# Kernel optimization log

Hardware: AMD Instinct MI355X
Metric: run time of the kernel (lower is better)

## Reference

```python
import jax, jax.numpy as jnp
import numpy as np

N = 262144   # collocation points
Q = 100      # IRK stages
H = 50       # hidden width (hardcoded in DNN)


def setup_inputs() -> dict:
    key = jax.random.key(0)
    ks = jax.random.split(key, 16)
    dims = [(1, H), (H, H), (H, H), (H, H), (H, H), (H, Q)]
    inp = {}
    for j, (i, o) in enumerate(dims):
        k1, k2 = jax.random.split(ks[j])
        s = 1.0 / np.sqrt(i)  # torch nn.Linear default init range
        inp[f"W{j}"] = jax.random.uniform(k1, (i, o), jnp.float32, -s, s)
        inp[f"b{j}"] = jax.random.uniform(k2, (o,), jnp.float32, -s, s)
    inp["x"] = jax.random.uniform(ks[10], (N, 1), jnp.float32, -1.0, 1.0)
    inp["lambda_1"] = jnp.array([0.0], jnp.float32)
    inp["lambda_2"] = jnp.array([-6.0], jnp.float32)
    inp["IRK_alpha"] = jax.random.uniform(ks[11], (Q, Q), jnp.float32) * 0.01
    inp["dt"] = jnp.float32(0.01)
    return inp


def reference(W0, b0, W1, b1, W2, b2, W3, b3, W4, b4, W5, b5,
              x, lambda_1, lambda_2, IRK_alpha, dt):
    def u_fn(xx):  # [N,1] -> [N,Q]
        h = xx
        for W, b in ((W0, b0), (W1, b1), (W2, b2), (W3, b3), (W4, b4)):
            h = jnp.tanh(h @ W + b)
        return h @ W5 + b5

    ones = jnp.ones_like(x)
    # u_x, u_xx via nested forward-mode (x is scalar per sample, so jvp with
    # tangent 1 gives the exact per-column derivative, same as the torch
    # double-autograd dummy trick).
    def u_and_ux(xx):
        return jax.jvp(u_fn, (xx,), (ones,))  # (u, u_x)

    (u, u_x), (_, u_xx) = jax.jvp(u_and_ux, (x,), (ones,))

    f = -lambda_1 * u * u_x + jnp.exp(lambda_2) * u_xx  # [N,Q]
    return u - dt * (f @ IRK_alpha.T)
```

## Files before the change

### kernel.cpp

```cpp
#include <hip/hip_runtime.h>
#include <hip/hip_bf16.h>


#define NPTS 262144
#define HW   50
#define Q    100
#define BLK  64
#define SPW  32
#define SPB  32
#define NBLK (NPTS / SPB)

#define WS_W5    65536
#define WS_W5AF  94208
#define WS_ALPHA 108544
#define WS_DENSE 137216

typedef float f32x4 __attribute__((ext_vector_type(4)));
typedef short bf16x8 __attribute__((ext_vector_type(8)));
typedef unsigned int u32x4 __attribute__((ext_vector_type(4)));

#define MFMA __builtin_amdgcn_mfma_f32_16x16x32_bf16

__device__ __forceinline__ unsigned int pack_bf2(float a, float b) {
    __hip_bfloat162 h = __float22bfloat162_rn(make_float2(a, b));
    unsigned int u;
    __builtin_memcpy(&u, &h, 4);
    return u;
}
__device__ __forceinline__ float lo_f(unsigned int p) {
    return __builtin_bit_cast(float, p << 16);
}
__device__ __forceinline__ float hi_f(unsigned int p) {
    return __builtin_bit_cast(float, p & 0xffff0000u);
}
__device__ __forceinline__ float fast_tanh(float z) {
    float e = __expf(2.0f * z);
    return 1.0f - __fdividef(2.0f, e + 1.0f);
}

__global__ void __launch_bounds__(256, 1)
compute_w5a(const float* __restrict__ W5, const float* __restrict__ alpha,
            float* __restrict__ w5a)
{
    int idx = blockIdx.x * 256 + threadIdx.x;
    if (idx >= HW * Q) return;
    int i = idx / Q, q = idx - i * Q;
    float acc = 0.0f;
    for (int j = 0; j < Q; ++j)
        acc = fmaf(W5[i * Q + j], alpha[q * Q + j], acc);
    w5a[idx] = acc;
}

__global__ void __launch_bounds__(64, 1)
build_frags(const float* __restrict__ W1, const float* __restrict__ W2,
            const float* __restrict__ W3, const float* __restrict__ W4,
            const float* __restrict__ W5, const float* __restrict__ alpha,
            unsigned char* __restrict__ ws)
{
    const int ln  = threadIdx.x;
    const int fid = blockIdx.x;

    const float* src;
    int ld, kmax, mmax, kt, mt;
    bool trans, isLo;
    size_t dst;

    if (fid < 64) {
        int L = fid >> 4, f = fid & 15;
        src = (L == 0) ? W1 : (L == 1) ? W2 : (L == 2) ? W3 : W4;
        ld = HW; kmax = HW; mmax = HW; trans = true;
        isLo = f >= 8;
        int ff = f & 7;
        kt = ff >> 2; mt = ff & 3;
        dst = (size_t)(L * 16384 + f * 1024);
    } else if (fid < 92) {
        int f = fid - 64;
        src = W5; ld = Q; kmax = HW; mmax = Q; trans = true;
        isLo = f >= 14;
        int ff = isLo ? f - 14 : f;
        kt = ff / 7; mt = ff % 7;
        dst = (size_t)(WS_W5 + f * 1024);
    } else if (fid < 106) {
        int f = fid - 92;
        src = (const float*)(ws + WS_DENSE);
        ld = Q; kmax = HW; mmax = Q; trans = true;
        isLo = false;
        kt = f / 7; mt = f % 7;
        dst = (size_t)(WS_W5AF + f * 1024);
    } else {
        int f = fid - 106;
        src = alpha; ld = Q; kmax = Q; mmax = Q; trans = false;
        isLo = false;
        kt = f / 7; mt = f % 7;
        dst = (size_t)(WS_ALPHA + f * 1024);
    }

    int m  = mt * 16 + (ln & 15);
    int kb = kt * 32 + (ln >> 4) * 8;
    bool mv = (m < mmax);
    unsigned int wout[4];
#pragma unroll
    for (int jj = 0; jj < 4; ++jj) {
        int k0 = kb + 2 * jj, k1 = k0 + 1;
        float v0 = (mv && k0 < kmax) ? (trans ? src[k0 * ld + m] : src[m * ld + k0]) : 0.0f;
        float v1 = (mv && k1 < kmax) ? (trans ? src[k1 * ld + m] : src[m * ld + k1]) : 0.0f;
        unsigned int h = pack_bf2(v0, v1);
        if (isLo)
            wout[jj] = pack_bf2(v0 - lo_f(h), v1 - hi_f(h));
        else
            wout[jj] = h;
    }
    *(uint4*)(ws + dst + ln * 16) = make_uint4(wout[0], wout[1], wout[2], wout[3]);
}

__global__ void __launch_bounds__(BLK, 2)
pinn_mfma(const float* __restrict__ b0v, const float* __restrict__ W0,
          const float* __restrict__ b1, const float* __restrict__ b2,
          const float* __restrict__ b3, const float* __restrict__ b4,
          const float* __restrict__ b5,
          const float* __restrict__ x, const float* __restrict__ lam1p,
          const float* __restrict__ lam2p, const float* __restrict__ dtp,
          const unsigned char* __restrict__ ws, float* __restrict__ out)
{
    __shared__ __align__(16) unsigned char statebuf[8192];

    const int lane = threadIdx.x & 63;
    const int l15  = lane & 15;
    const int g    = lane >> 4;
    const int sbase = blockIdx.x * SPB;

    unsigned char* st0 = &statebuf[0];
    unsigned char* st1 = &statebuf[4096];
    const unsigned char* wgl = ws + lane * 16;
    const int swz = (l15 & 7) << 4;

    const f32x4 Z4 = {0.0f, 0.0f, 0.0f, 0.0f};

    bf16x8 Bh_hi[2][2], Bh_lo[2][2], Bx[2][2], Bxx[2][2];

    {
        float xv[2];
        xv[0] = x[sbase + l15];
        xv[1] = x[sbase + 16 + l15];
#pragma unroll
        for (int kt = 0; kt < 2; ++kt) {
            float wv[8], bv[8];
#pragma unroll
            for (int j = 0; j < 8; ++j) {
                int ch = kt * 32 + g * 8 + j;
                wv[j] = (ch < HW) ? W0[ch] : 0.0f;
                bv[j] = (ch < HW) ? b0v[ch] : 0.0f;
            }
#pragma unroll
            for (int nt = 0; nt < 2; ++nt) {
                u32x4 uh, ul, ux, uxx;
#pragma unroll
                for (int jp = 0; jp < 4; ++jp) {
                    float t0 = fast_tanh(fmaf(xv[nt], wv[2*jp],   bv[2*jp]));
                    float t1 = fast_tanh(fmaf(xv[nt], wv[2*jp+1], bv[2*jp+1]));
                    float s0 = 1.0f - t0 * t0, s1 = 1.0f - t1 * t1;
                    float hx0 = s0 * wv[2*jp],   hx1 = s1 * wv[2*jp+1];
                    float hxx0 = -2.0f * t0 * hx0 * wv[2*jp];
                    float hxx1 = -2.0f * t1 * hx1 * wv[2*jp+1];
                    unsigned int h = pack_bf2(t0, t1);
                    uh[jp]  = h;
                    ul[jp]  = pack_bf2(t0 - lo_f(h), t1 - hi_f(h));
                    ux[jp]  = pack_bf2(hx0, hx1);
                    uxx[jp] = pack_bf2(hxx0, hxx1);
                }
                Bh_hi[kt][nt] = __builtin_bit_cast(bf16x8, uh);
                Bh_lo[kt][nt] = __builtin_bit_cast(bf16x8, ul);
                Bx[kt][nt]    = __builtin_bit_cast(bf16x8, ux);
                Bxx[kt][nt]   = __builtin_bit_cast(bf16x8, uxx);
            }
        }
    }

    for (int L = 0; L < 4; ++L) {
        const float* bl = (L == 0) ? b1 : (L == 1) ? b2 : (L == 2) ? b3 : b4;
        const unsigned char* wfl = wgl + L * 16384;

        float bb[4][4];
#pragma unroll
        for (int mt = 0; mt < 4; ++mt)
#pragma unroll
            for (int r = 0; r < 4; ++r) {
                int ch = mt * 16 + g * 4 + r;
                bb[mt][r] = (ch < HW) ? bl[ch] : 0.0f;
            }

        f32x4 at[4][2], ax[4][2], axx[4][2];
#pragma unroll
        for (int mt = 0; mt < 4; ++mt)
#pragma unroll
            for (int nt = 0; nt < 2; ++nt) {
#pragma unroll
                for (int r = 0; r < 4; ++r) at[mt][nt][r] = bb[mt][r];
                ax[mt][nt] = Z4; axx[mt][nt] = Z4;
            }

#pragma unroll
        for (int kt = 0; kt < 2; ++kt) {
#pragma unroll
            for (int mt = 0; mt < 4; ++mt) {
                bf16x8 Ahi = *(const bf16x8*)(wfl + (kt * 4 + mt) * 1024);
                bf16x8 Alo = *(const bf16x8*)(wfl + (8 + kt * 4 + mt) * 1024);
#pragma unroll
                for (int nt = 0; nt < 2; ++nt) {
                    at[mt][nt]  = MFMA(Ahi, Bh_hi[kt][nt], at[mt][nt], 0, 0, 0);
                    at[mt][nt]  = MFMA(Ahi, Bh_lo[kt][nt], at[mt][nt], 0, 0, 0);
                    at[mt][nt]  = MFMA(Alo, Bh_hi[kt][nt], at[mt][nt], 0, 0, 0);
                    ax[mt][nt]  = MFMA(Ahi, Bx[kt][nt],  ax[mt][nt],  0, 0, 0);
                    axx[mt][nt] = MFMA(Ahi, Bxx[kt][nt], axx[mt][nt], 0, 0, 0);
                }
            }
        }

#pragma unroll
        for (int mt = 0; mt < 4; ++mt)
#pragma unroll
            for (int nt = 0; nt < 2; ++nt) {
                float t0 = fast_tanh(at[mt][nt][0]);
                float t1 = fast_tanh(at[mt][nt][1]);
                float t2 = fast_tanh(at[mt][nt][2]);
                float t3 = fast_tanh(at[mt][nt][3]);
                at[mt][nt][0] = t0; at[mt][nt][1] = t1;
                at[mt][nt][2] = t2; at[mt][nt][3] = t3;
                unsigned int h0 = pack_bf2(t0, t1);
                unsigned int h1 = pack_bf2(t2, t3);
                unsigned int l0 = pack_bf2(t0 - lo_f(h0), t1 - hi_f(h0));
                unsigned int l1 = pack_bf2(t2 - lo_f(h1), t3 - hi_f(h1));
                int off = ((nt * 16 + l15) * 128 + (mt * 16 + g * 4) * 2) ^ swz;
                *(uint2*)(st0 + off) = make_uint2(h0, h1);
                *(uint2*)(st1 + off) = make_uint2(l0, l1);
            }
#pragma unroll
        for (int kt = 0; kt < 2; ++kt)
#pragma unroll
            for (int nt = 0; nt < 2; ++nt) {
                int off = ((nt * 16 + l15) * 128 + (kt * 32 + g * 8) * 2) ^ swz;
                Bh_hi[kt][nt] = *(const bf16x8*)(st0 + off);
                Bh_lo[kt][nt] = *(const bf16x8*)(st1 + off);
            }
        asm volatile("s_waitcnt lgkmcnt(0)" ::: "memory");

#pragma unroll
        for (int mt = 0; mt < 4; ++mt)
#pragma unroll
            for (int nt = 0; nt < 2; ++nt) {
                float hx[4], hxx[4];
#pragma unroll
                for (int r = 0; r < 4; ++r) {
                    float t   = at[mt][nt][r];
                    float s   = fmaf(-t, t, 1.0f);
                    float zx  = ax[mt][nt][r];
                    float zxx = axx[mt][nt][r];
                    hx[r]  = s * zx;
                    hxx[r] = fmaf(s, zxx, -2.0f * t * zx * hx[r]);
                }
                unsigned int a0 = pack_bf2(hx[0], hx[1]);
                unsigned int a1 = pack_bf2(hx[2], hx[3]);
                unsigned int c0 = pack_bf2(hxx[0], hxx[1]);
                unsigned int c1 = pack_bf2(hxx[2], hxx[3]);
                int off = ((nt * 16 + l15) * 128 + (mt * 16 + g * 4) * 2) ^ swz;
                *(uint2*)(st0 + off) = make_uint2(a0, a1);
                *(uint2*)(st1 + off) = make_uint2(c0, c1);
            }
#pragma unroll
        for (int kt = 0; kt < 2; ++kt)
#pragma unroll
            for (int nt = 0; nt < 2; ++nt) {
                int off = ((nt * 16 + l15) * 128 + (kt * 32 + g * 8) * 2) ^ swz;
                Bx[kt][nt]  = *(const bf16x8*)(st0 + off);
                Bxx[kt][nt] = *(const bf16x8*)(st1 + off);
            }
        asm volatile("s_waitcnt lgkmcnt(0)" ::: "memory");
    }

    const float lam1 = lam1p[0];
    const float el2  = __expf(lam2p[0]);
    const float dtv  = dtp[0];

    const unsigned char* w5f = wgl + WS_W5;

    if (lam1 == 0.0f) {
        const unsigned char* waf = wgl + WS_W5AF;
        const float c = dtv * el2;
#pragma unroll
        for (int mt = 0; mt < 7; ++mt) {
            f32x4 au[2], acr[2];
#pragma unroll
            for (int nt = 0; nt < 2; ++nt) {
#pragma unroll
                for (int r = 0; r < 4; ++r) {
                    int q = mt * 16 + g * 4 + r;
                    au[nt][r] = (q < Q) ? b5[q] : 0.0f;
                }
                acr[nt] = Z4;
            }
#pragma unroll
            for (int kt = 0; kt < 2; ++kt) {
                bf16x8 Ahi = *(const bf16x8*)(w5f + (kt * 7 + mt) * 1024);
                bf16x8 Alo = *(const bf16x8*)(w5f + (14 + kt * 7 + mt) * 1024);
                bf16x8 Aa  = *(const bf16x8*)(waf + (kt * 7 + mt) * 1024);
#pragma unroll
                for (int nt = 0; nt < 2; ++nt) {
                    au[nt]  = MFMA(Ahi, Bh_hi[kt][nt], au[nt],  0, 0, 0);
                    au[nt]  = MFMA(Ahi, Bh_lo[kt][nt], au[nt],  0, 0, 0);
                    au[nt]  = MFMA(Alo, Bh_hi[kt][nt], au[nt],  0, 0, 0);
                    acr[nt] = MFMA(Aa,  Bxx[kt][nt],   acr[nt], 0, 0, 0);
                }
            }
#pragma unroll
            for (int nt = 0; nt < 2; ++nt) {
                int s = nt * 16 + l15;
                f32x4 ov;
#pragma unroll
                for (int r = 0; r < 4; ++r)
                    ov[r] = fmaf(-c, acr[nt][r], au[nt][r]);
                *(f32x4*)(st0 + s * 64 + g * 16) = ov;
            }
            asm volatile("s_waitcnt lgkmcnt(0)" ::: "memory");
#pragma unroll
            for (int p = 0; p < 2; ++p) {
                int s  = p * 16 + (lane >> 2);
                int qi = (lane & 3) * 4;
                f32x4 v = *(const f32x4*)(st0 + s * 64 + qi * 4);
                int qb = mt * 16 + qi;
                if (qb < Q)
                    *(f32x4*)(&out[(size_t)(sbase + s) * Q + qb]) = v;
            }
            asm volatile("s_waitcnt lgkmcnt(0)" ::: "memory");
        }
    } else {
        f32x4 u_all[7][2];
#pragma unroll
        for (int mt = 0; mt < 7; ++mt) {
            f32x4 au[2], aux_[2], auxx[2];
#pragma unroll
            for (int nt = 0; nt < 2; ++nt) {
#pragma unroll
                for (int r = 0; r < 4; ++r) {
                    int q = mt * 16 + g * 4 + r;
                    au[nt][r] = (q < Q) ? b5[q] : 0.0f;
                }
                aux_[nt] = Z4; auxx[nt] = Z4;
            }
#pragma unroll
            for (int kt = 0; kt < 2; ++kt) {
                bf16x8 Ahi = *(const bf16x8*)(w5f + (kt * 7 + mt) * 1024);
                bf16x8 Alo = *(const bf16x8*)(w5f + (14 + kt * 7 + mt) * 1024);
#pragma unroll
                for (int nt = 0; nt < 2; ++nt) {
                    au[nt]   = MFMA(Ahi, Bh_hi[kt][nt], au[nt],   0, 0, 0);
                    au[nt]   = MFMA(Ahi, Bh_lo[kt][nt], au[nt],   0, 0, 0);
                    au[nt]   = MFMA(Alo, Bh_hi[kt][nt], au[nt],   0, 0, 0);
                    aux_[nt] = MFMA(Ahi, Bx[kt][nt],  aux_[nt], 0, 0, 0);
                    auxx[nt] = MFMA(Ahi, Bxx[kt][nt], auxx[nt], 0, 0, 0);
                }
            }
#pragma unroll
            for (int nt = 0; nt < 2; ++nt) {
                float fv[4];
#pragma unroll
                for (int r = 0; r < 4; ++r) {
                    int q = mt * 16 + g * 4 + r;
                    float u = au[nt][r];
                    u_all[mt][nt][r] = u;
                    float f = fmaf(-lam1 * u, aux_[nt][r], el2 * auxx[nt][r]);
                    fv[r] = (q < Q) ? f : 0.0f;
                }
                unsigned int f0 = pack_bf2(fv[0], fv[1]);
                unsigned int f1 = pack_bf2(fv[2], fv[3]);
                int s = nt * 16 + l15;
                int off = (s * 256 + (mt * 16 + g * 4) * 2) ^ swz;
                *(uint2*)(st0 + off) = make_uint2(f0, f1);
            }
        }

        bf16x8 Ff[4][2];
#pragma unroll
        for (int kt = 0; kt < 4; ++kt)
#pragma unroll
            for (int nt = 0; nt < 2; ++nt) {
                int s = nt * 16 + l15;
                int off = (s * 256 + (kt * 32 + g * 8) * 2) ^ swz;
                Ff[kt][nt] = *(const bf16x8*)(st0 + off);
            }
        asm volatile("s_waitcnt lgkmcnt(0)" ::: "memory");
        {
            const bf16x8 z8 = {0, 0, 0, 0, 0, 0, 0, 0};
            if (g >= 2) { Ff[3][0] = z8; Ff[3][1] = z8; }
        }

        const unsigned char* alf = wgl + WS_ALPHA;
#pragma unroll
        for (int mt = 0; mt < 7; ++mt) {
            f32x4 ac[2]; ac[0] = Z4; ac[1] = Z4;
#pragma unroll
            for (int kt = 0; kt < 4; ++kt) {
                bf16x8 Aa = *(const bf16x8*)(alf + (kt * 7 + mt) * 1024);
#pragma unroll
                for (int nt = 0; nt < 2; ++nt)
                    ac[nt] = MFMA(Aa, Ff[kt][nt], ac[nt], 0, 0, 0);
            }
#pragma unroll
            for (int nt = 0; nt < 2; ++nt) {
                int s = nt * 16 + l15;
                f32x4 ov;
#pragma unroll
                for (int r = 0; r < 4; ++r)
                    ov[r] = fmaf(-dtv, ac[nt][r], u_all[mt][nt][r]);
                *(f32x4*)(st0 + s * 64 + g * 16) = ov;
            }
            asm volatile("s_waitcnt lgkmcnt(0)" ::: "memory");
#pragma unroll
            for (int p = 0; p < 2; ++p) {
                int s  = p * 16 + (lane >> 2);
                int qi = (lane & 3) * 4;
                f32x4 v = *(const f32x4*)(st0 + s * 64 + qi * 4);
                int qb = mt * 16 + qi;
                if (qb < Q)
                    *(f32x4*)(&out[(size_t)(sbase + s) * Q + qb]) = v;
            }
            asm volatile("s_waitcnt lgkmcnt(0)" ::: "memory");
        }
    }
}

extern "C" void kernel_launch(void* const* d_in, const int* in_sizes, int n_in,
                              void* d_out, int out_size, void* d_ws, size_t ws_size,
                              hipStream_t stream) {
    const float* W0 = (const float*)d_in[0];
    const float* b0 = (const float*)d_in[1];
    const float* W1 = (const float*)d_in[2];
    const float* b1 = (const float*)d_in[3];
    const float* W2 = (const float*)d_in[4];
    const float* b2 = (const float*)d_in[5];
    const float* W3 = (const float*)d_in[6];
    const float* b3 = (const float*)d_in[7];
    const float* W4 = (const float*)d_in[8];
    const float* b4 = (const float*)d_in[9];
    const float* W5 = (const float*)d_in[10];
    const float* b5 = (const float*)d_in[11];
    const float* x     = (const float*)d_in[12];
    const float* lam1  = (const float*)d_in[13];
    const float* lam2  = (const float*)d_in[14];
    const float* alpha = (const float*)d_in[15];
    const float* dt    = (const float*)d_in[16];

    unsigned char* ws = (unsigned char*)d_ws;

    compute_w5a<<<20, 256, 0, stream>>>(W5, alpha, (float*)(ws + WS_DENSE));
    build_frags<<<134, 64, 0, stream>>>(W1, W2, W3, W4, W5, alpha, ws);
    pinn_mfma<<<NBLK, BLK, 0, stream>>>(b0, W0, b1, b2, b3, b4, b5,
                                        x, lam1, lam2, dt,
                                        (const unsigned char*)ws, (float*)d_out);
}
```

Measured before the change: 124.7 us.

## Restructure hidden layers per M-tile with four LDS staging buffers

Reorders each hidden layer so every 16-channel M-tile does its MFMAs, tanh and derivative epilogue before the next tile starts. This cuts live accumulators from 24 f32x4 to 6 and lowers register pressure. The h, h_lo, h_x and h_xx tiles now go to four separate LDS buffers, doubling shared memory to 16KB, and are reloaded with a single wait instead of two. The extra LDS per block could limit occupancy, and the per-tile MFMA chains are shorter with less independent work to interleave.

```diff
diff --git a/kernel.cpp b/kernel.cpp
--- a/kernel.cpp
+++ b/kernel.cpp
@@ -122,15 +122,17 @@
           const float* __restrict__ lam2p, const float* __restrict__ dtp,
           const unsigned char* __restrict__ ws, float* __restrict__ out)
 {
-    __shared__ __align__(16) unsigned char statebuf[8192];
+    __shared__ __align__(16) unsigned char statebuf[16384];
 
     const int lane = threadIdx.x & 63;
     const int l15  = lane & 15;
     const int g    = lane >> 4;
     const int sbase = blockIdx.x * SPB;
 
-    unsigned char* st0 = &statebuf[0];
-    unsigned char* st1 = &statebuf[4096];
+    unsigned char* stHh  = &statebuf[0];
+    unsigned char* stHl  = &statebuf[4096];
+    unsigned char* stHx  = &statebuf[8192];
+    unsigned char* stHxx = &statebuf[12288];
     const unsigned char* wgl = ws + lane * 16;
     const int swz = (l15 & 7) << 4;
 
@@ -180,99 +182,68 @@
         const float* bl = (L == 0) ? b1 : (L == 1) ? b2 : (L == 2) ? b3 : b4;
         const unsigned char* wfl = wgl + L * 16384;
 
-        float bb[4][4];
-#pragma unroll
-        for (int mt = 0; mt < 4; ++mt)
-#pragma unroll
-            for (int r = 0; r < 4; ++r) {
-                int ch = mt * 16 + g * 4 + r;
-                bb[mt][r] = (ch < HW) ? bl[ch] : 0.0f;
-            }
-
-        f32x4 at[4][2], ax[4][2], axx[4][2];
-#pragma unroll
-        for (int mt = 0; mt < 4; ++mt)
-#pragma unroll
-            for (int nt = 0; nt < 2; ++nt) {
-#pragma unroll
-                for (int r = 0; r < 4; ++r) at[mt][nt][r] = bb[mt][r];
-                ax[mt][nt] = Z4; axx[mt][nt] = Z4;
-            }
-
-#pragma unroll
-        for (int kt = 0; kt < 2; ++kt) {
-#pragma unroll
-            for (int mt = 0; mt < 4; ++mt) {
+#pragma unroll
+        for (int mt = 0; mt < 4; ++mt) {
+            f32x4 at[2], ax[2], axx[2];
+#pragma unroll
+            for (int nt = 0; nt < 2; ++nt) {
+#pragma unroll
+                for (int r = 0; r < 4; ++r) {
+                    int ch = mt * 16 + g * 4 + r;
+                    at[nt][r] = (ch < HW) ? bl[ch] : 0.0f;
+                }
+                ax[nt] = Z4; axx[nt] = Z4;
+            }
+#pragma unroll
+            for (int kt = 0; kt < 2; ++kt) {
                 bf16x8 Ahi = *(const bf16x8*)(wfl + (kt * 4 + mt) * 1024);
                 bf16x8 Alo = *(const bf16x8*)(wfl + (8 + kt * 4 + mt) * 1024);
 #pragma unroll
                 for (int nt = 0; nt < 2; ++nt) {
-                    at[mt][nt]  = MFMA(Ahi, Bh_hi[kt][nt], at[mt][nt], 0, 0, 0);
-                    at[mt][nt]  = MFMA(Ahi, Bh_lo[kt][nt], at[mt][nt], 0, 0, 0);
-                    at[mt][nt]  = MFMA(Alo, Bh_hi[kt][nt], at[mt][nt], 0, 0, 0);
-                    ax[mt][nt]  = MFMA(Ahi, Bx[kt][nt],  ax[mt][nt],  0, 0, 0);
-                    axx[mt][nt] = MFMA(Ahi, Bxx[kt][nt], axx[mt][nt], 0, 0, 0);
-                }
-            }
-        }
-
-#pragma unroll
-        for (int mt = 0; mt < 4; ++mt)
-#pragma unroll
-            for (int nt = 0; nt < 2; ++nt) {
-                float t0 = fast_tanh(at[mt][nt][0]);
-                float t1 = fast_tanh(at[mt][nt][1]);
-                float t2 = fast_tanh(at[mt][nt][2]);
-                float t3 = fast_tanh(at[mt][nt][3]);
-                at[mt][nt][0] = t0; at[mt][nt][1] = t1;
-                at[mt][nt][2] = t2; at[mt][nt][3] = t3;
-                unsigned int h0 = pack_bf2(t0, t1);
-                unsigned int h1 = pack_bf2(t2, t3);
-                unsigned int l0 = pack_bf2(t0 - lo_f(h0), t1 - hi_f(h0));
-                unsigned int l1 = pack_bf2(t2 - lo_f(h1), t3 - hi_f(h1));
-                int off = ((nt * 16 + l15) * 128 + (mt * 16 + g * 4) * 2) ^ swz;
-                *(uint2*)(st0 + off) = make_uint2(h0, h1);
-                *(uint2*)(st1 + off) = make_uint2(l0, l1);
-            }
-#pragma unroll
-        for (int kt = 0; kt < 2; ++kt)
-#pragma unroll
-            for (int nt = 0; nt < 2; ++nt) {
-                int off = ((nt * 16 + l15) * 128 + (kt * 32 + g * 8) * 2) ^ swz;
-                Bh_hi[kt][nt] = *(const bf16x8*)(st0 + off);
-                Bh_lo[kt][nt] = *(const bf16x8*)(st1 + off);
-            }
-        asm volatile("s_waitcnt lgkmcnt(0)" ::: "memory");
-
-#pragma unroll
-        for (int mt = 0; mt < 4; ++mt)
-#pragma unroll
-            for (int nt = 0; nt < 2; ++nt) {
-                float hx[4], hxx[4];
+                    at[nt]  = MFMA(Ahi, Bh_hi[kt][nt], at[nt],  0, 0, 0);
+                    at[nt]  = MFMA(Ahi, Bh_lo[kt][nt], at[nt],  0, 0, 0);
+                    at[nt]  = MFMA(Alo, Bh_hi[kt][nt], at[nt],  0, 0, 0);
+                    ax[nt]  = MFMA(Ahi, Bx[kt][nt],  ax[nt],  0, 0, 0);
+                    axx[nt] = MFMA(Ahi, Bxx[kt][nt], axx[nt], 0, 0, 0);
+                }
+            }
+#pragma unroll
+            for (int nt = 0; nt < 2; ++nt) {
+                float t[4], hx[4], hxx[4];
 #pragma unroll
                 for (int r = 0; r < 4; ++r) {
-                    float t   = at[mt][nt][r];
-                    float s   = fmaf(-t, t, 1.0f);
-                    float zx  = ax[mt][nt][r];
-                    float zxx = axx[mt][nt][r];
+                    float tv  = fast_tanh(at[nt][r]);
+                    float s   = fmaf(-tv, tv, 1.0f);
+                    float zx  = ax[nt][r];
+                    float zxx = axx[nt][r];
+                    t[r]   = tv;
                     hx[r]  = s * zx;
-                    hxx[r] = fmaf(s, zxx, -2.0f * t * zx * hx[r]);
-                }
+                    hxx[r] = fmaf(s, zxx, -2.0f * tv * zx * hx[r]);
+                }
+                unsigned int h0 = pack_bf2(t[0], t[1]);
+                unsigned int h1 = pack_bf2(t[2], t[3]);
+                unsigned int l0 = pack_bf2(t[0] - lo_f(h0), t[1] - hi_f(h0));
+                unsigned int l1 = pack_bf2(t[2] - lo_f(h1), t[3] - hi_f(h1));
                 unsigned int a0 = pack_bf2(hx[0], hx[1]);
                 unsigned int a1 = pack_bf2(hx[2], hx[3]);
                 unsigned int c0 = pack_bf2(hxx[0], hxx[1]);
                 unsigned int c1 = pack_bf2(hxx[2], hxx[3]);
                 int off = ((nt * 16 + l15) * 128 + (mt * 16 + g * 4) * 2) ^ swz;
-                *(uint2*)(st0 + off) = make_uint2(a0, a1);
-                *(uint2*)(st1 + off) = make_uint2(c0, c1);
-            }
+                *(uint2*)(stHh  + off) = make_uint2(h0, h1);
+                *(uint2*)(stHl  + off) = make_uint2(l0, l1);
+                *(uint2*)(stHx  + off) = make_uint2(a0, a1);
+                *(uint2*)(stHxx + off) = make_uint2(c0, c1);
+            }
+        }
 #pragma unroll
         for (int kt = 0; kt < 2; ++kt)
 #pragma unroll
             for (int nt = 0; nt < 2; ++nt) {
                 int off = ((nt * 16 + l15) * 128 + (kt * 32 + g * 8) * 2) ^ swz;
-                Bx[kt][nt]  = *(const bf16x8*)(st0 + off);
-                Bxx[kt][nt] = *(const bf16x8*)(st1 + off);
+                Bh_hi[kt][nt] = *(const bf16x8*)(stHh  + off);
+                Bh_lo[kt][nt] = *(const bf16x8*)(stHl  + off);
+                Bx[kt][nt]    = *(const bf16x8*)(stHx  + off);
+                Bxx[kt][nt]   = *(const bf16x8*)(stHxx + off);
             }
         asm volatile("s_waitcnt lgkmcnt(0)" ::: "memory");
     }
@@ -282,6 +253,7 @@
     const float dtv  = dtp[0];
 
     const unsigned char* w5f = wgl + WS_W5;
+    unsigned char* st0 = stHh;
 
     if (lam1 == 0.0f) {
         const unsigned char* waf = wgl + WS_W5AF;
```

Measured after the change: 127.4 us. 1.02x slower.
